# Kernel tuning notes

Measured on AMD Instinct MI355X. Metric: run time of the kernel, lower is better.

## Reference

```python
import jax, jax.numpy as jnp
import numpy as np
import itertools, math

METRIC = [1.0, 1.0, 1.0]  # Cl(3,0)
EPS = 1e-6
SQRT2 = math.sqrt(2.0)


def _build_algebra(metric):
    d = len(metric)
    # basis blades ordered by grade, then lexicographic combination (repo convention)
    blades = []
    for g in range(d + 1):
        for c in itertools.combinations(range(d), g):
            blades.append(sum(1 << i for i in c))
    idx = {m: i for i, m in enumerate(blades)}
    n = len(blades)
    C = np.zeros((n, n, n), dtype=np.float32)  # cayley[i, j, k]: e_i * e_k -> sign * e_j
    for ia, am in enumerate(blades):
        for ik, bm in enumerate(blades):
            a = am >> 1
            swaps = 0
            while a:
                swaps += bin(a & bm).count('1')
                a >>= 1
            sign = -1.0 if (swaps & 1) else 1.0
            for i in range(d):
                if am & bm & (1 << i):
                    sign *= metric[i]
            C[ia, idx[am ^ bm], ik] = sign
    grades = np.array([bin(m).count('1') for m in blades])
    subspaces = np.array([int((grades == g).sum()) for g in range(d + 1)])
    paths = np.zeros((d + 1, d + 1, d + 1), dtype=bool)
    for i in range(d + 1):
        for j in range(d + 1):
            for k in range(d + 1):
                paths[i, j, k] = np.any(C[np.ix_(grades == i, grades == j, grades == k)] != 0)
    return C, subspaces, paths, grades

CAYLEY_NP, SUBSPACES, PATHS, GRADE_OF_COMP = _build_algebra(METRIC)
REP_IDX = np.repeat(np.arange(len(SUBSPACES)), SUBSPACES)  # component -> grade, len 8
PI, PJ, PK = np.nonzero(PATHS)                              # 20 active grade triples
ONEHOT_GRADE = np.eye(len(SUBSPACES), dtype=np.float32)[GRADE_OF_COMP]  # [8,4]

B, N_IN, N_OUT = 1024, 256, 256
DIM_MV = CAYLEY_NP.shape[0]  # 8
N_PATHS = int(PATHS.sum())   # 20


def mv_linear(x, w, bias=None):
    # MVLinear: per-grade weight repeated over components; einsum 'bm...i,nmi->bn...i'
    wr = w[:, :, REP_IDX]                       # [out, in, 8]
    out = jnp.einsum('bmi,nmi->bni', x, wr)
    if bias is not None:
        out = out.at[:, :, 0].add(bias[:, :, 0])  # bias embedded in scalar (grade-0) slot
    return out


def normalize_mv(x, a):
    # per-grade norms (Euclidean metric => L2 norm of each grade block)
    oh = jnp.asarray(ONEHOT_GRADE)
    norms = jnp.sqrt(jnp.einsum('bni,ig->bng', x * x, oh))  # [b, n, 4]
    interp = jax.nn.sigmoid(a)[None] * (norms - 1.0) + 1.0  # learned interp toward unit norm
    return x / (interp[:, :, REP_IDX] + EPS)


def gp_kernel(gp_weight):
    # scatter 20 path weights into (m, n, 4, 4, 4), repeat per subspace, mask by cayley
    m, n, _ = gp_weight.shape
    g = len(SUBSPACES)
    w4 = jnp.zeros((m, n, g, g, g), gp_weight.dtype).at[:, :, PI, PJ, PK].set(gp_weight)
    wrep = w4[:, :, REP_IDX][:, :, :, REP_IDX][:, :, :, :, REP_IDX]  # [m, n, 8, 8, 8]
    return jnp.asarray(CAYLEY_NP)[None, None] * wrep


def setup_inputs() -> dict:
    key = jax.random.key(0)
    ks = jax.random.split(key, 5)
    std_gp = 1.0 / math.sqrt(N_IN * (len(METRIC) + 1))
    std_lin = 1.0 / math.sqrt(N_IN)
    return {
        'x': jax.random.normal(ks[0], (B, N_IN, DIM_MV), jnp.float32),
        'w_right': jax.random.normal(ks[1], (N_IN, N_IN, len(SUBSPACES)), jnp.float32) * std_lin,
        'w_left': jax.random.normal(ks[2], (N_OUT, N_IN, len(SUBSPACES)), jnp.float32) * std_lin,
        'b_left': jax.random.normal(ks[3], (1, N_OUT, 1), jnp.float32) * 0.02,
        'norm_a': jnp.zeros((N_IN, len(SUBSPACES)), jnp.float32),  # normalization_init = 0
        'gp_weight': jax.random.normal(ks[4], (N_OUT, N_IN, N_PATHS), jnp.float32) * std_gp,
    }


def reference(x, w_right, w_left, b_left, norm_a, gp_weight):
    x_right = normalize_mv(mv_linear(x, w_right), norm_a)
    kernel = gp_kernel(gp_weight)                 # [m, n, 8, 8, 8]
    outer = jnp.einsum('bni,bnk->bnik', x, x_right)  # [b, n, 8, 8]
    prod = jnp.einsum('bnik,mnijk->bmj', outer, kernel)
    left = mv_linear(x, w_left, b_left)
    return (left + prod) / SQRT2
```

## Files before the change

### kernel.cpp

```cpp
#include <hip/hip_runtime.h>
#include <math.h>

typedef unsigned short ushortT;
typedef __bf16 bf16x8 __attribute__((ext_vector_type(8)));
typedef float  f32x4  __attribute__((ext_vector_type(4)));

__constant__ int GRADEc[8] = {0,1,1,1,2,2,2,3};

__constant__ int CMAPc[8][7] = {
  {0, 8, 9,10,11, 0, 0},
  {1,12,13,14,15,16,17},
  {2,18,19,20,21,22,23},
  {3,24,25,26,27,28,29},
  {4,30,31,32,33,34,35},
  {5,36,37,38,39,40,41},
  {6,42,43,44,45,46,47},
  {7,48,49,50,51, 0, 0}};
__constant__ int WMAPc[8][7] = {
  {0, 4, 8,14,20, 0, 0},
  {1, 5, 9,10,15,16,21},
  {1, 5, 9,10,15,16,21},
  {1, 5, 9,10,15,16,21},
  {2, 6,11,12,17,18,22},
  {2, 6,11,12,17,18,22},
  {2, 6,11,12,17,18,22},
  {3, 7,13,19,23, 0, 0}};
__constant__ int NSLOTc[8] = {5,7,7,7,7,7,7,5};
__constant__ int SSTARTc[8][4] = {
  {0,2,3,4},{0,2,4,6},{0,2,4,6},{0,2,4,6},
  {0,2,4,6},{0,2,4,6},{0,2,4,6},{0,2,3,4}};
__constant__ int SCOUNTc[8][4] = {
  {2,1,1,1},{2,2,2,1},{2,2,2,1},{2,2,2,1},
  {2,2,2,1},{2,2,2,1},{2,2,2,1},{2,1,1,1}};

__device__ __forceinline__ ushortT f2bf(float f) {
  unsigned int u = __float_as_uint(f);
  unsigned int r = (u + 0x7fffu + ((u >> 16) & 1u)) >> 16;
  return (ushortT)r;
}

#define GLOAD_LDS16(gsrc, ldst) \
  __builtin_amdgcn_global_load_lds((const __attribute__((address_space(1))) unsigned int*)(gsrc), \
                                   (__attribute__((address_space(3))) unsigned int*)(ldst), 16, 0, 0)

#define WAITVM(N) asm volatile("s_waitcnt vmcnt(" #N ")" ::: "memory")
#define SCHEDB()  __builtin_amdgcn_sched_barrier(0)
#define RAWBAR()  do { SCHEDB(); __builtin_amdgcn_s_barrier(); asm volatile("" ::: "memory"); SCHEDB(); } while (0)

__global__ void k_prep(const float* __restrict__ x, const float* __restrict__ w_right,
                       const float* __restrict__ w_left, const float* __restrict__ gp,
                       ushortT* __restrict__ XH, ushortT* __restrict__ XL,
                       ushortT* __restrict__ WH, ushortT* __restrict__ WL,
                       ushortT* __restrict__ WT2b) {
  const int bid = blockIdx.x;
  const int tid = threadIdx.x;
  if (bid < 6144) {
    int t = bid * 256 + tid;
    int n = t & 255, m = (t >> 8) & 255, w = t >> 16;
    float v = (w < 4) ? w_left[m * 1024 + n * 4 + w] : gp[m * 5120 + n * 20 + (w - 4)];
    WT2b[t] = f2bf(v);
  } else if (bid < 7168) {
    int b = bid - 6144;
    const float4* xp = (const float4*)(x + b * 2048 + tid * 8);
    float4 a = xp[0], c = xp[1];
    float v[8] = {a.x, a.y, a.z, a.w, c.x, c.y, c.z, c.w};
    #pragma unroll
    for (int i = 0; i < 8; ++i) {
      ushortT h = f2bf(v[i]);
      float hf = __uint_as_float(((unsigned int)h) << 16);
      XH[i * 262144 + b * 256 + tid] = h;
      XL[i * 262144 + b * 256 + tid] = f2bf(v[i] - hf);
    }
  } else {
    int n = bid - 7168;
    float4 w = *(const float4*)(w_right + n * 1024 + tid * 4);
    float v[4] = {w.x, w.y, w.z, w.w};
    #pragma unroll
    for (int g = 0; g < 4; ++g) {
      ushortT h = f2bf(v[g]);
      float hf = __uint_as_float(((unsigned int)h) << 16);
      WH[g * 65536 + n * 256 + tid] = h;
      WL[g * 65536 + n * 256 + tid] = f2bf(v[g] - hf);
    }
  }
}

__global__ __launch_bounds__(512) void k_right_feat(const ushortT* __restrict__ XH,
                                                    const ushortT* __restrict__ XL,
                                                    const ushortT* __restrict__ WH,
                                                    const ushortT* __restrict__ WL,
                                                    const float* __restrict__ x,
                                                    const float* __restrict__ norm_a,
                                                    ushortT* __restrict__ FT2b) {
  const int lin = blockIdx.x;
  const int rr  = lin & 7;
  const int q   = lin >> 3;
  const int xb  = q & 7;
  const int yb  = (q >> 3) * 8 + rr;
  const int n0 = xb * 32;
  const int b0 = yb * 32;
  __shared__ __align__(16) ushortT lds[49152];
  const int t    = threadIdx.x;
  const int wave = t >> 6;
  const int lane = t & 63;
  const int i    = wave;
  const int g    = GRADEc[i];
  const int lrow = lane & 15, lkg = lane >> 4;
  const int srow = lane >> 2;
  const int sseg = lane & 3;

  const ushortT* Asrc_h = XH + i * 262144 + b0 * 256;
  const ushortT* Asrc_l = XL + i * 262144 + b0 * 256;
  const int bg = wave >> 1;
  const ushortT* Bsrc = ((wave & 1) ? WL : WH) + bg * 65536 + n0 * 256;

  f32x4 acc[2][2];
  #pragma unroll
  for (int r = 0; r < 2; ++r)
    #pragma unroll
    for (int c = 0; c < 2; ++c)
      acc[r][c] = (f32x4){0.f, 0.f, 0.f, 0.f};

  auto STAGE = [&](int k0, int buf) {
    ushortT* base = lds + buf * 24576;
    #pragma unroll
    for (int q2 = 0; q2 < 2; ++q2) {
      int row = q2 * 16 + srow;
      int slog = sseg ^ ((row >> 1) & 3);
      GLOAD_LDS16(Asrc_h + row * 256 + k0 + slog * 8, base + i * 1024 + q2 * 512);
      GLOAD_LDS16(Asrc_l + row * 256 + k0 + slog * 8, base + 8192 + i * 1024 + q2 * 512);
      GLOAD_LDS16(Bsrc   + row * 256 + k0 + slog * 8,
                  base + 16384 + (wave & 1) * 4096 + bg * 1024 + q2 * 512);
    }
  };

  auto COMPUTE = [&](int buf) {
    const ushortT* base = lds + buf * 24576;
    bf16x8 afh[2], afl[2], bfh[2], bfl[2];
    #pragma unroll
    for (int r = 0; r < 2; ++r) {
      int row = r * 16 + lrow;
      int po = row * 32 + (lkg ^ ((row >> 1) & 3)) * 8;
      afh[r] = *(const bf16x8*)(base + i * 1024 + po);
      afl[r] = *(const bf16x8*)(base + 8192 + i * 1024 + po);
    }
    #pragma unroll
    for (int c = 0; c < 2; ++c) {
      int row = c * 16 + lrow;
      int po = row * 32 + (lkg ^ ((row >> 1) & 3)) * 8;
      bfh[c] = *(const bf16x8*)(base + 16384 + g * 1024 + po);
      bfl[c] = *(const bf16x8*)(base + 20480 + g * 1024 + po);
    }
    #pragma unroll
    for (int r = 0; r < 2; ++r)
      #pragma unroll
      for (int c = 0; c < 2; ++c) {
        acc[r][c] = __builtin_amdgcn_mfma_f32_16x16x32_bf16(afh[r], bfh[c], acc[r][c], 0, 0, 0);
        acc[r][c] = __builtin_amdgcn_mfma_f32_16x16x32_bf16(afl[r], bfh[c], acc[r][c], 0, 0, 0);
        acc[r][c] = __builtin_amdgcn_mfma_f32_16x16x32_bf16(afh[r], bfl[c], acc[r][c], 0, 0, 0);
      }
  };

  STAGE(0, 0);
  int cur = 0;
  for (int tc = 0; tc < 8; ++tc) {
    if (tc < 7) { STAGE((tc + 1) * 32, cur ^ 1); SCHEDB(); WAITVM(6); }
    else        { WAITVM(0); }
    RAWBAR();
    COMPUTE(cur);
    if (tc < 7) RAWBAR();
    cur ^= 1;
  }

  float* yl = (float*)lds;
  #pragma unroll
  for (int r = 0; r < 2; ++r)
    #pragma unroll
    for (int c = 0; c < 2; ++c)
      #pragma unroll
      for (int e = 0; e < 4; ++e) {
        int row = r * 16 + lkg * 4 + e;
        int col = c * 16 + lrow;
        yl[i * 1056 + row * 33 + col] = acc[r][c][e];
      }
  __syncthreads();

  #pragma unroll
  for (int e2 = 0; e2 < 2; ++e2) {
    int el  = t + e2 * 512;
    int row = el >> 5, col = el & 31;
    int b = b0 + row, n = n0 + col;
    float y[8];
    #pragma unroll
    for (int q2 = 0; q2 < 8; ++q2) y[q2] = yl[q2 * 1056 + row * 33 + col];
    const float4* xp = (const float4*)(x + b * 2048 + n * 8);
    float4 x01 = xp[0], x23 = xp[1];
    float xv[8] = {x01.x, x01.y, x01.z, x01.w, x23.x, x23.y, x23.z, x23.w};
    float4 na = *(const float4*)(norm_a + n * 4);
    float nav[4] = {na.x, na.y, na.z, na.w};
    float nr[4];
    nr[0] = fabsf(y[0]);
    nr[1] = sqrtf(y[1]*y[1] + y[2]*y[2] + y[3]*y[3]);
    nr[2] = sqrtf(y[4]*y[4] + y[5]*y[5] + y[6]*y[6]);
    nr[3] = fabsf(y[7]);
    float inv[4];
    #pragma unroll
    for (int gg = 0; gg < 4; ++gg) {
      float s = 1.0f / (1.0f + expf(-nav[gg]));
      inv[gg] = 1.0f / (s * (nr[gg] - 1.0f) + 1.0f + 1e-6f);
    }
    float r[8];
    r[0] = y[0]*inv[0];
    r[1] = y[1]*inv[1]; r[2] = y[2]*inv[1]; r[3] = y[3]*inv[1];
    r[4] = y[4]*inv[2]; r[5] = y[5]*inv[2]; r[6] = y[6]*inv[2];
    r[7] = y[7]*inv[3];

    float F[52];
    F[8]  = xv[0]*r[0];
    F[9]  = xv[1]*r[1] + xv[2]*r[2] + xv[3]*r[3];
    F[10] = -(xv[4]*r[4] + xv[5]*r[5] + xv[6]*r[6]);
    F[11] = -xv[7]*r[7];
    F[12] = xv[0]*r[1];
    F[13] = xv[1]*r[0];
    F[14] = -(xv[2]*r[4] + xv[3]*r[5]);
    F[15] = xv[4]*r[2] + xv[5]*r[3];
    F[16] = -xv[6]*r[7];
    F[17] = -xv[7]*r[6];
    F[18] = xv[0]*r[2];
    F[19] = xv[2]*r[0];
    F[20] = xv[1]*r[4] - xv[3]*r[6];
    F[21] = -xv[4]*r[1] + xv[6]*r[3];
    F[22] = xv[5]*r[7];
    F[23] = xv[7]*r[5];
    F[24] = xv[0]*r[3];
    F[25] = xv[3]*r[0];
    F[26] = xv[1]*r[5] + xv[2]*r[6];
    F[27] = -(xv[5]*r[1] + xv[6]*r[2]);
    F[28] = -xv[4]*r[7];
    F[29] = -xv[7]*r[4];
    F[30] = xv[0]*r[4];
    F[31] = xv[1]*r[2] - xv[2]*r[1];
    F[32] = xv[3]*r[7];
    F[33] = xv[4]*r[0];
    F[34] = -xv[5]*r[6] + xv[6]*r[5];
    F[35] = xv[7]*r[3];
    F[36] = xv[0]*r[5];
    F[37] = xv[1]*r[3] - xv[3]*r[1];
    F[38] = -xv[2]*r[7];
    F[39] = xv[5]*r[0];
    F[40] = xv[4]*r[6] - xv[6]*r[4];
    F[41] = -xv[7]*r[2];
    F[42] = xv[0]*r[6];
    F[43] = xv[2]*r[3] - xv[3]*r[2];
    F[44] = xv[1]*r[7];
    F[45] = xv[6]*r[0];
    F[46] = -xv[4]*r[5] + xv[5]*r[4];
    F[47] = xv[7]*r[1];
    F[48] = xv[0]*r[7];
    F[49] = xv[1]*r[6] - xv[2]*r[5] + xv[3]*r[4];
    F[50] = xv[4]*r[3] - xv[5]*r[2] + xv[6]*r[1];
    F[51] = xv[7]*r[0];

    #pragma unroll
    for (int c = 8; c < 52; ++c)
      FT2b[c * 262144 + b * 256 + n] = f2bf(F[c]);
  }
}

__global__ __launch_bounds__(256) void k_gemm_mfma(const ushortT* __restrict__ XH,
                                                   const ushortT* __restrict__ FT2b,
                                                   const ushortT* __restrict__ WT2b,
                                                   float* __restrict__ outP) {
  const int lin = blockIdx.x;
  const int rr  = lin & 7;
  const int q   = lin >> 3;
  const int ix  = q & 15;
  const int z   = (q >> 4) * 8 + rr;
  const int j   = z >> 2;
  const int ks  = z & 3;
  const int m0  = (ix & 1) * 128;
  const int b0  = (ix >> 1) * 128;
  __shared__ __align__(16) ushortT lds[32768];
  const int t    = threadIdx.x;
  const int wave = t >> 6;
  const int lane = t & 63;
  const int wb   = (wave & 1) * 64;
  const int wm   = (wave >> 1) * 64;
  const int lrow = lane & 15;
  const int lkg  = lane >> 4;
  const int srow = lane >> 3;
  const int sseg = lane & 7;

  f32x4 acc[4][4];
  #pragma unroll
  for (int r = 0; r < 4; ++r)
    #pragma unroll
    for (int c = 0; c < 4; ++c)
      acc[r][c] = (f32x4){0.f, 0.f, 0.f, 0.f};

  const int sstart = SSTARTc[j][ks];
  const int nt     = SCOUNTc[j][ks] * 4;

  auto STAGE = [&](int tch, int buf) {
    int slot = sstart + (tch >> 2);
    int k0   = (tch & 3) << 6;
    const ushortT* Ap = ((slot == 0) ? (XH + j * 262144)
                                     : (FT2b + CMAPc[j][slot] * 262144)) + b0 * 256;
    const ushortT* Bp = WT2b + WMAPc[j][slot] * 65536 + m0 * 256;
    #pragma unroll
    for (int q2 = 0; q2 < 4; ++q2) {
      int idx = wave * 4 + q2;
      int row = idx * 8 + srow;
      int slog = sseg ^ (row & 7);
      GLOAD_LDS16(Ap + row * 256 + k0 + slog * 8, lds + buf * 8192 + idx * 512);
      GLOAD_LDS16(Bp + row * 256 + k0 + slog * 8, lds + 16384 + buf * 8192 + idx * 512);
    }
  };

  STAGE(0, 0);
  int cur = 0;
  for (int tc = 0; tc < nt; ++tc) {
    if (tc + 1 < nt) { STAGE(tc + 1, cur ^ 1); SCHEDB(); WAITVM(8); }
    else             { WAITVM(0); }
    RAWBAR();
    const ushortT* sA = lds + cur * 8192;
    const ushortT* sB = lds + 16384 + cur * 8192;
    #pragma unroll
    for (int kk = 0; kk < 2; ++kk) {
      bf16x8 af[4], bf[4];
      #pragma unroll
      for (int r = 0; r < 4; ++r) {
        int row = wb + r * 16 + lrow;
        af[r] = *(const bf16x8*)(sA + row * 64 + (((kk * 4 + lkg) ^ (row & 7)) * 8));
      }
      #pragma unroll
      for (int c = 0; c < 4; ++c) {
        int row = wm + c * 16 + lrow;
        bf[c] = *(const bf16x8*)(sB + row * 64 + (((kk * 4 + lkg) ^ (row & 7)) * 8));
      }
      #pragma unroll
      for (int r = 0; r < 4; ++r)
        #pragma unroll
        for (int c = 0; c < 4; ++c)
          acc[r][c] = __builtin_amdgcn_mfma_f32_16x16x32_bf16(af[r], bf[c], acc[r][c], 0, 0, 0);
    }
    if (tc + 1 < nt) RAWBAR();
    cur ^= 1;
  }

  float* oj = outP + (ks * 8 + j) * 262144;
  #pragma unroll
  for (int r = 0; r < 4; ++r) {
    #pragma unroll
    for (int c = 0; c < 4; ++c) {
      #pragma unroll
      for (int e = 0; e < 4; ++e) {
        int brow = b0 + wb + r * 16 + lkg * 4 + e;
        int mcol = m0 + wm + c * 16 + lrow;
        oj[brow * 256 + mcol] = acc[r][c][e];
      }
    }
  }
}

__global__ void k_merge(const float* __restrict__ outP, const float* __restrict__ bleft,
                        float* __restrict__ out) {
  const int t4 = (blockIdx.x * 256 + threadIdx.x) * 4;
  const int m  = t4 & 255;
  const float sc = 0.7071067811865475f;
  float o[4][8];
  #pragma unroll
  for (int jj = 0; jj < 8; ++jj) {
    float4 s = make_float4(0.f, 0.f, 0.f, 0.f);
    #pragma unroll
    for (int p = 0; p < 4; ++p) {
      float4 v = *(const float4*)(outP + (p * 8 + jj) * 262144 + t4);
      s.x += v.x; s.y += v.y; s.z += v.z; s.w += v.w;
    }
    o[0][jj] = s.x; o[1][jj] = s.y; o[2][jj] = s.z; o[3][jj] = s.w;
  }
  #pragma unroll
  for (int q = 0; q < 4; ++q) {
    float ov[8];
    #pragma unroll
    for (int jj = 0; jj < 8; ++jj) ov[jj] = o[q][jj];
    ov[0] += bleft[m + q];
    float4 v0 = make_float4(ov[0]*sc, ov[1]*sc, ov[2]*sc, ov[3]*sc);
    float4 v1 = make_float4(ov[4]*sc, ov[5]*sc, ov[6]*sc, ov[7]*sc);
    *(float4*)(out + (t4 + q) * 8)     = v0;
    *(float4*)(out + (t4 + q) * 8 + 4) = v1;
  }
}

extern "C" void kernel_launch(void* const* d_in, const int* in_sizes, int n_in,
                              void* d_out, int out_size, void* d_ws, size_t ws_size,
                              hipStream_t stream) {
  const float* x       = (const float*)d_in[0];
  const float* w_right = (const float*)d_in[1];
  const float* w_left  = (const float*)d_in[2];
  const float* b_left  = (const float*)d_in[3];
  const float* norm_a  = (const float*)d_in[4];
  const float* gp      = (const float*)d_in[5];
  float* out = (float*)d_out;
  float* W   = (float*)d_ws;

  float*   outP = W;
  ushortT* XH   = (ushortT*)(W + 8388608);
  ushortT* XL   = (ushortT*)(W + 9437184);
  ushortT* WH   = (ushortT*)(W + 10485760);
  ushortT* WL   = (ushortT*)(W + 10616832);
  ushortT* FT2b = (ushortT*)(W + 10747904);
  ushortT* WT2b = (ushortT*)(W + 17563648);

  k_prep<<<7424, 256, 0, stream>>>(x, w_right, w_left, gp, XH, XL, WH, WL, WT2b);
  k_right_feat<<<256, 512, 0, stream>>>(XH, XL, WH, WL, x, norm_a, FT2b);
  k_gemm_mfma<<<512, 256, 0, stream>>>(XH, FT2b, WT2b, outP);
  k_merge<<<256, 256, 0, stream>>>(outP, b_left, out);
}
```

Measured before the change: 116.5 us.

## Halve split-K partials, use intra-block K split across waves, vectorize weight prep

The GEMM kernel now uses 512-thread blocks where two groups of four waves each handle half of every 64-wide K chunk, and the two groups' accumulators are reduced through LDS before the store. The outer split-K drops from four partial slices to two, so half as many fp32 partials are written and k_merge reads half as much. The weight-conversion part of k_prep is rewritten so each thread reads w_left and gp rows with float4 loads instead of scattered scalar gathers, which cuts the prep grid. The trade-off is fewer blocks (256) and longer per-block K loops, plus an extra LDS reduction step.

Result: faster. 109.9 us, median of 2 (-5.6%).

```diff
diff --git a/kernel.cpp b/kernel.cpp
--- a/kernel.cpp
+++ b/kernel.cpp
@@ -25,13 +25,8 @@
   {2, 6,11,12,17,18,22},
   {2, 6,11,12,17,18,22},
   {3, 7,13,19,23, 0, 0}};
-__constant__ int NSLOTc[8] = {5,7,7,7,7,7,7,5};
-__constant__ int SSTARTc[8][4] = {
-  {0,2,3,4},{0,2,4,6},{0,2,4,6},{0,2,4,6},
-  {0,2,4,6},{0,2,4,6},{0,2,4,6},{0,2,3,4}};
-__constant__ int SCOUNTc[8][4] = {
-  {2,1,1,1},{2,2,2,1},{2,2,2,1},{2,2,2,1},
-  {2,2,2,1},{2,2,2,1},{2,2,2,1},{2,1,1,1}};
+__constant__ int SSTART2c[8][2] = {{0,3},{0,4},{0,4},{0,4},{0,4},{0,4},{0,4},{0,3}};
+__constant__ int SCOUNT2c[8][2] = {{3,2},{4,3},{4,3},{4,3},{4,3},{4,3},{4,3},{3,2}};
 
 __device__ __forceinline__ ushortT f2bf(float f) {
   unsigned int u = __float_as_uint(f);
@@ -54,13 +49,26 @@
                        ushortT* __restrict__ WT2b) {
   const int bid = blockIdx.x;
   const int tid = threadIdx.x;
-  if (bid < 6144) {
-    int t = bid * 256 + tid;
-    int n = t & 255, m = (t >> 8) & 255, w = t >> 16;
-    float v = (w < 4) ? w_left[m * 1024 + n * 4 + w] : gp[m * 5120 + n * 20 + (w - 4)];
-    WT2b[t] = f2bf(v);
-  } else if (bid < 7168) {
-    int b = bid - 6144;
+  if (bid < 256) {
+    const int m = bid, n = tid;
+    float4 wl = *(const float4*)(w_left + m * 1024 + n * 4);
+    float g[20];
+    const float4* gp4 = (const float4*)(gp + m * 5120 + n * 20);
+    #pragma unroll
+    for (int q = 0; q < 5; ++q) {
+      float4 v = gp4[q];
+      g[q * 4 + 0] = v.x; g[q * 4 + 1] = v.y; g[q * 4 + 2] = v.z; g[q * 4 + 3] = v.w;
+    }
+    const int base = m * 256 + n;
+    WT2b[0 * 65536 + base] = f2bf(wl.x);
+    WT2b[1 * 65536 + base] = f2bf(wl.y);
+    WT2b[2 * 65536 + base] = f2bf(wl.z);
+    WT2b[3 * 65536 + base] = f2bf(wl.w);
+    #pragma unroll
+    for (int p = 0; p < 20; ++p)
+      WT2b[(4 + p) * 65536 + base] = f2bf(g[p]);
+  } else if (bid < 1280) {
+    int b = bid - 256;
     const float4* xp = (const float4*)(x + b * 2048 + tid * 8);
     float4 a = xp[0], c = xp[1];
     float v[8] = {a.x, a.y, a.z, a.w, c.x, c.y, c.z, c.w};
@@ -72,15 +80,15 @@
       XL[i * 262144 + b * 256 + tid] = f2bf(v[i] - hf);
     }
   } else {
-    int n = bid - 7168;
+    int n = bid - 1280;
     float4 w = *(const float4*)(w_right + n * 1024 + tid * 4);
     float v[4] = {w.x, w.y, w.z, w.w};
     #pragma unroll
-    for (int g = 0; g < 4; ++g) {
-      ushortT h = f2bf(v[g]);
+    for (int g2 = 0; g2 < 4; ++g2) {
+      ushortT h = f2bf(v[g2]);
       float hf = __uint_as_float(((unsigned int)h) << 16);
-      WH[g * 65536 + n * 256 + tid] = h;
-      WL[g * 65536 + n * 256 + tid] = f2bf(v[g] - hf);
+      WH[g2 * 65536 + n * 256 + tid] = h;
+      WL[g2 * 65536 + n * 256 + tid] = f2bf(v[g2] - hf);
     }
   }
 }
@@ -267,7 +275,7 @@
   }
 }
 
-__global__ __launch_bounds__(256) void k_gemm_mfma(const ushortT* __restrict__ XH,
+__global__ __launch_bounds__(512) void k_gemm_mfma(const ushortT* __restrict__ XH,
                                                    const ushortT* __restrict__ FT2b,
                                                    const ushortT* __restrict__ WT2b,
                                                    float* __restrict__ outP) {
@@ -275,17 +283,19 @@
   const int rr  = lin & 7;
   const int q   = lin >> 3;
   const int ix  = q & 15;
-  const int z   = (q >> 4) * 8 + rr;
-  const int j   = z >> 2;
-  const int ks  = z & 3;
+  const int z   = rr + 8 * (q >> 4);
+  const int j   = z >> 1;
+  const int ks  = z & 1;
   const int m0  = (ix & 1) * 128;
   const int b0  = (ix >> 1) * 128;
   __shared__ __align__(16) ushortT lds[32768];
   const int t    = threadIdx.x;
   const int wave = t >> 6;
+  const int kkg  = wave >> 2;
+  const int w4   = wave & 3;
   const int lane = t & 63;
-  const int wb   = (wave & 1) * 64;
-  const int wm   = (wave >> 1) * 64;
+  const int wb   = (w4 & 1) * 64;
+  const int wm   = (w4 >> 1) * 64;
   const int lrow = lane & 15;
   const int lkg  = lane >> 4;
   const int srow = lane >> 3;
@@ -298,8 +308,8 @@
     for (int c = 0; c < 4; ++c)
       acc[r][c] = (f32x4){0.f, 0.f, 0.f, 0.f};
 
-  const int sstart = SSTARTc[j][ks];
-  const int nt     = SCOUNTc[j][ks] * 4;
+  const int sstart = SSTART2c[j][ks];
+  const int nt     = SCOUNT2c[j][ks] * 4;
 
   auto STAGE = [&](int tch, int buf) {
     int slot = sstart + (tch >> 2);
@@ -308,8 +318,8 @@
                                      : (FT2b + CMAPc[j][slot] * 262144)) + b0 * 256;
     const ushortT* Bp = WT2b + WMAPc[j][slot] * 65536 + m0 * 256;
     #pragma unroll
-    for (int q2 = 0; q2 < 4; ++q2) {
-      int idx = wave * 4 + q2;
+    for (int q2 = 0; q2 < 2; ++q2) {
+      int idx = wave * 2 + q2;
       int row = idx * 8 + srow;
       int slog = sseg ^ (row & 7);
       GLOAD_LDS16(Ap + row * 256 + k0 + slog * 8, lds + buf * 8192 + idx * 512);
@@ -320,44 +330,59 @@
   STAGE(0, 0);
   int cur = 0;
   for (int tc = 0; tc < nt; ++tc) {
-    if (tc + 1 < nt) { STAGE(tc + 1, cur ^ 1); SCHEDB(); WAITVM(8); }
+    if (tc + 1 < nt) { STAGE(tc + 1, cur ^ 1); SCHEDB(); WAITVM(4); }
     else             { WAITVM(0); }
     RAWBAR();
     const ushortT* sA = lds + cur * 8192;
     const ushortT* sB = lds + 16384 + cur * 8192;
-    #pragma unroll
-    for (int kk = 0; kk < 2; ++kk) {
-      bf16x8 af[4], bf[4];
+    bf16x8 af[4], bf[4];
+    #pragma unroll
+    for (int r = 0; r < 4; ++r) {
+      int row = wb + r * 16 + lrow;
+      af[r] = *(const bf16x8*)(sA + row * 64 + (((kkg * 4 + lkg) ^ (row & 7)) * 8));
+    }
+    #pragma unroll
+    for (int c = 0; c < 4; ++c) {
+      int row = wm + c * 16 + lrow;
+      bf[c] = *(const bf16x8*)(sB + row * 64 + (((kkg * 4 + lkg) ^ (row & 7)) * 8));
+    }
+    #pragma unroll
+    for (int r = 0; r < 4; ++r)
       #pragma unroll
-      for (int r = 0; r < 4; ++r) {
-        int row = wb + r * 16 + lrow;
-        af[r] = *(const bf16x8*)(sA + row * 64 + (((kk * 4 + lkg) ^ (row & 7)) * 8));
-      }
+      for (int c = 0; c < 4; ++c)
+        acc[r][c] = __builtin_amdgcn_mfma_f32_16x16x32_bf16(af[r], bf[c], acc[r][c], 0, 0, 0);
+    if (tc + 1 < nt) RAWBAR();
+    cur ^= 1;
+  }
+
+  __syncthreads();
+  float* fl = (float*)lds;
+  if (kkg == 1) {
+    #pragma unroll
+    for (int r = 0; r < 4; ++r)
+      #pragma unroll
+      for (int c = 0; c < 4; ++c)
+        #pragma unroll
+        for (int e = 0; e < 4; ++e) {
+          int row = r * 16 + lkg * 4 + e;
+          int col = c * 16 + lrow;
+          fl[w4 * 4096 + row * 64 + col] = acc[r][c][e];
+        }
+  }
+  __syncthreads();
+  if (kkg == 0) {
+    float* oj = outP + (ks * 8 + j) * 262144;
+    #pragma unroll
+    for (int r = 0; r < 4; ++r) {
       #pragma unroll
       for (int c = 0; c < 4; ++c) {
-        int row = wm + c * 16 + lrow;
-        bf[c] = *(const bf16x8*)(sB + row * 64 + (((kk * 4 + lkg) ^ (row & 7)) * 8));
-      }
-      #pragma unroll
-      for (int r = 0; r < 4; ++r)
         #pragma unroll
-        for (int c = 0; c < 4; ++c)
-          acc[r][c] = __builtin_amdgcn_mfma_f32_16x16x32_bf16(af[r], bf[c], acc[r][c], 0, 0, 0);
-    }
-    if (tc + 1 < nt) RAWBAR();
-    cur ^= 1;
-  }
-
-  float* oj = outP + (ks * 8 + j) * 262144;
-  #pragma unroll
-  for (int r = 0; r < 4; ++r) {
-    #pragma unroll
-    for (int c = 0; c < 4; ++c) {
-      #pragma unroll
-      for (int e = 0; e < 4; ++e) {
-        int brow = b0 + wb + r * 16 + lkg * 4 + e;
-        int mcol = m0 + wm + c * 16 + lrow;
-        oj[brow * 256 + mcol] = acc[r][c][e];
+        for (int e = 0; e < 4; ++e) {
+          int row = r * 16 + lkg * 4 + e;
+          int col = c * 16 + lrow;
+          float v = acc[r][c][e] + fl[w4 * 4096 + row * 64 + col];
+          oj[(b0 + wb + row) * 256 + m0 + wm + col] = v;
+        }
       }
     }
   }
@@ -373,7 +398,7 @@
   for (int jj = 0; jj < 8; ++jj) {
     float4 s = make_float4(0.f, 0.f, 0.f, 0.f);
     #pragma unroll
-    for (int p = 0; p < 4; ++p) {
+    for (int p = 0; p < 2; ++p) {
       float4 v = *(const float4*)(outP + (p * 8 + jj) * 262144 + t4);
       s.x += v.x; s.y += v.y; s.z += v.z; s.w += v.w;
     }
@@ -405,15 +430,15 @@
   float* W   = (float*)d_ws;
 
   float*   outP = W;
-  ushortT* XH   = (ushortT*)(W + 8388608);
-  ushortT* XL   = (ushortT*)(W + 9437184);
-  ushortT* WH   = (ushortT*)(W + 10485760);
-  ushortT* WL   = (ushortT*)(W + 10616832);
-  ushortT* FT2b = (ushortT*)(W + 10747904);
-  ushortT* WT2b = (ushortT*)(W + 17563648);
-
-  k_prep<<<7424, 256, 0, stream>>>(x, w_right, w_left, gp, XH, XL, WH, WL, WT2b);
+  ushortT* XH   = (ushortT*)(W + 4194304);
+  ushortT* XL   = (ushortT*)(W + 5242880);
+  ushortT* WH   = (ushortT*)(W + 6291456);
+  ushortT* WL   = (ushortT*)(W + 6422528);
+  ushortT* FT2b = (ushortT*)(W + 6553600);
+  ushortT* WT2b = (ushortT*)(W + 13369344);
+
+  k_prep<<<1536, 256, 0, stream>>>(x, w_right, w_left, gp, XH, XL, WH, WL, WT2b);
   k_right_feat<<<256, 512, 0, stream>>>(XH, XL, WH, WL, x, norm_a, FT2b);
-  k_gemm_mfma<<<512, 256, 0, stream>>>(XH, FT2b, WT2b, outP);
+  k_gemm_mfma<<<256, 512, 0, stream>>>(XH, FT2b, WT2b, outP);
   k_merge<<<256, 256, 0, stream>>>(outP, b_left, out);
 }
```
